# Performance work log

Hardware: AMD Instinct MI355X
Metric: run time of the kernel (lower is better)

The kernel has to match this reference:

```python
import jax, jax.numpy as jnp
import numpy as np

B, N, C, H, M, T, L = 2, 4096, 256, 8, 48, 10000, 256
CH = C // H
HID = 512  # mlp_ratio=2


def _ln(x, g, b, eps=1e-5):
    mu = x.mean(-1, keepdims=True)
    var = ((x - mu) ** 2).mean(-1, keepdims=True)
    return (x - mu) * jax.lax.rsqrt(var + eps) * g + b


def setup_inputs() -> dict:
    key = jax.random.key(0)
    ks = iter(jax.random.split(key, 40))
    nrm = lambda shape, s=0.02: jax.random.normal(next(ks), shape, jnp.float32) * s
    return dict(
        feat=jax.random.normal(next(ks), (B, N, C), jnp.float32),
        memory=jax.random.normal(next(ks), (B, L, C), jnp.float32),
        member_idx=jax.random.randint(next(ks), (B, N, M), 0, N),
        cluster_mask=jax.random.randint(next(ks), (B, N, M), 0, 2, jnp.int32),
        pe_idx=jax.random.randint(next(ks), (B, N, M), 0, T),
        global_attn=0,
        pre_table=jax.random.normal(next(ks), (T, 5), jnp.float32),
        Wq=nrm((C, C)), bq=jnp.zeros(C), Wkv=nrm((C, 2 * C)), bkv=jnp.zeros(2 * C),
        blank_k=nrm((C,), 1.0), blank_v=nrm((C,), 1.0),
        Wpe=nrm((5, H)), bpe=jnp.zeros(H),
        Wproj=nrm((C, C)), bproj=jnp.zeros(C),
        g1=jnp.ones(C), be1=jnp.zeros(C), g2=jnp.ones(C), be2=jnp.zeros(C),
        xWq=nrm((C, C)), xbq=jnp.zeros(C), xWk=nrm((C, C)), xbk=jnp.zeros(C),
        xWv=nrm((C, C)), xbv=jnp.zeros(C), xWo=nrm((C, C)), xbo=jnp.zeros(C),
        xg=jnp.ones(C), xbe=jnp.zeros(C),
        W1=nrm((C, HID)), bf1=jnp.zeros(HID), W2=nrm((HID, C)), bf2=jnp.zeros(C),
    )


def _cluster_attn(x, member_idx, cluster_mask, pe_idx, pre_table,
                  Wq, bq, Wkv, bkv, blank_k, blank_v, Wpe, bpe, Wproj, bproj):
    b, n, c = x.shape
    scale = CH ** -0.5
    q = ((x @ Wq + bq) * scale).reshape(b, n, H, CH).transpose(0, 2, 1, 3)  # bhnc
    kv = (x @ Wkv + bkv).reshape(b, n, H, 2, CH)
    k = kv[..., 0, :].transpose(0, 2, 1, 3)  # bhnc
    v = kv[..., 1, :].transpose(0, 2, 1, 3)  # bhnc
    # CLUSTENQK: gather per-token neighborhood keys, dot with q -> b h n m
    gather = jax.vmap(lambda t, idx: t[:, idx, :])  # (h,n,c),(n,m)->(h,n,m,c)
    k_g = gather(k, member_idx)
    attn = jnp.einsum('bhnc,bhnmc->bhnm', q, k_g)
    # positional embedding table lookup
    pe_table = pre_table @ Wpe + bpe                 # T x H
    pos = pe_table[pe_idx].transpose(0, 3, 1, 2)     # b h n m
    attn = attn + pos
    maskf = cluster_mask.astype(attn.dtype)[:, None]  # b 1 n m
    attn = attn + (1.0 - maskf) * -100.0
    blank_attn = jnp.einsum('bhnc,hc->bhn', q, blank_k.reshape(H, CH))[..., None]
    p = jax.nn.softmax(jnp.concatenate([attn, blank_attn], axis=-1), axis=-1)
    pa, pb = p[..., :-1], p[..., -1:]
    # CLUSTENAV: gather values, weighted sum
    v_g = gather(v, member_idx)
    out = jnp.einsum('bhnm,bhnmc->bhnc', pa, v_g)
    out = out + pb * blank_v.reshape(1, H, 1, CH)
    out = out.transpose(0, 2, 1, 3).reshape(b, n, c)
    return out @ Wproj + bproj


def _cross_attn(tgt, memory, xWq, xbq, xWk, xbk, xWv, xbv, xWo, xbo, xg, xbe):
    b, n, c = tgt.shape
    t2 = _ln(tgt, xg, xbe)  # normalize_before=True
    q = (t2 @ xWq + xbq).reshape(b, n, H, CH).transpose(0, 2, 1, 3) * (CH ** -0.5)
    k = (memory @ xWk + xbk).reshape(b, -1, H, CH).transpose(0, 2, 1, 3)
    v = (memory @ xWv + xbv).reshape(b, -1, H, CH).transpose(0, 2, 1, 3)
    p = jax.nn.softmax(jnp.einsum('bhnc,bhlc->bhnl', q, k), axis=-1)
    o = jnp.einsum('bhnl,bhlc->bhnc', p, v).transpose(0, 2, 1, 3).reshape(b, n, c)
    return tgt + (o @ xWo + xbo)


def reference(feat, memory, member_idx, cluster_mask, pe_idx, global_attn, pre_table,
              Wq, bq, Wkv, bkv, blank_k, blank_v, Wpe, bpe, Wproj, bproj,
              g1, be1, g2, be2,
              xWq, xbq, xWk, xbk, xWv, xbv, xWo, xbo, xg, xbe,
              W1, bf1, W2, bf2):
    # global_attn is a static flag; this reference covers the local-cluster path
    assert global_attn == 0
    # local cluster attention with pre-norm residual (drop_path/layer_scale disabled)
    feat = feat + _cluster_attn(_ln(feat, g1, be1), member_idx, cluster_mask, pe_idx,
                                pre_table, Wq, bq, Wkv, bkv, blank_k, blank_v,
                                Wpe, bpe, Wproj, bproj)
    # cross attention to memory (pre-norm, residual inside)
    feat = _cross_attn(feat, memory, xWq, xbq, xWk, xbk, xWv, xbv, xWo, xbo, xg, xbe)
    # MLP block
    h = jax.nn.gelu(_ln(feat, g2, be2) @ W1 + bf1, approximate=False)
    feat = feat + (h @ W2 + bf2)
    return feat
```

## Files before the change

kernel.cpp:

```cpp
#include <hip/hip_runtime.h>
#include <hip/hip_bf16.h>
#include <math.h>

#define BB 2
#define NN 4096
#define CC 256
#define HH 8
#define MM 48
#define TT 10000
#define LL 256
#define CHDIM 32
#define HIDD 512
#define ROWS (BB*NN)

typedef __attribute__((ext_vector_type(8))) short bf16x8;
typedef __attribute__((ext_vector_type(4))) float f32x4;

static __device__ __forceinline__ short f2bf(float x) {
    __hip_bfloat16 h = __float2bfloat16(x);
    return *reinterpret_cast<short*>(&h);
}
static __device__ __forceinline__ float bf2f(short s) {
    unsigned int u = ((unsigned int)(unsigned short)s) << 16;
    union { unsigned int u; float f; } c; c.u = u;
    return c.f;
}

__global__ void prep_misc_kernel(const float* __restrict__ pre, const float* __restrict__ Wpe,
                                 const float* __restrict__ bpe, float* __restrict__ pet,
                                 const float* __restrict__ bq, const float* __restrict__ bkv,
                                 const float* __restrict__ xbk, const float* __restrict__ xbv,
                                 const float* __restrict__ xbq, float scale,
                                 float* __restrict__ bqkv, float* __restrict__ xbkv,
                                 float* __restrict__ xbqS,
                                 const float* __restrict__ memory, __hip_bfloat16* __restrict__ memBf) {
    int bid = blockIdx.x, tid = threadIdx.x;
    if (bid < 313) {
        int i = bid * 256 + tid;
        if (i >= TT * HH) return;
        int t = i / HH, h = i % HH;
        float s = bpe[h];
        #pragma unroll
        for (int j = 0; j < 5; ++j) s += pre[t * 5 + j] * Wpe[j * HH + h];
        pet[i] = s;
    } else if (bid < 319) {
        int i = (bid - 313) * 256 + tid;
        if (i < 256) bqkv[i] = bq[i] * scale;
        else if (i < 768) bqkv[i] = bkv[i - 256];
        else if (i < 1024) xbkv[i - 768] = xbk[i - 768];
        else if (i < 1280) xbkv[256 + i - 1024] = xbv[i - 1024];
        else if (i < 1536) xbqS[i - 1280] = xbq[i - 1280] * scale;
    } else {
        int i = (bid - 319) * 256 + tid;
        if (i < 131072) memBf[i] = __float2bfloat16(memory[i]);
    }
}

struct WtDesc { const float* src; __hip_bfloat16* dst; int K; int N; int tile0; float scl; };
struct WtArgs { WtDesc d[9]; };
__global__ __launch_bounds__(256) void wtrans_kernel(WtArgs a) {
    __shared__ float tile[32][33];
    int bid = blockIdx.x;
    int mi = 0;
    #pragma unroll
    for (int i = 1; i < 9; ++i) if (bid >= a.d[i].tile0) mi = i;
    WtDesc dsc = a.d[mi];
    int t = bid - dsc.tile0;
    int tiles_n = dsc.N >> 5;
    int k0 = (t / tiles_n) * 32, n0 = (t % tiles_n) * 32;
    int tx = threadIdx.x & 31, ty = threadIdx.x >> 5;
    #pragma unroll
    for (int i = 0; i < 32; i += 8)
        tile[ty + i][tx] = dsc.src[(size_t)(k0 + ty + i) * dsc.N + n0 + tx];
    __syncthreads();
    #pragma unroll
    for (int i = 0; i < 32; i += 8)
        dsc.dst[(size_t)(n0 + ty + i) * dsc.K + k0 + tx] = __float2bfloat16(tile[tx][ty + i] * dsc.scl);
}

__global__ __launch_bounds__(256) void ln_kernel(const float* __restrict__ in,
                                                 const float* __restrict__ g,
                                                 const float* __restrict__ b,
                                                 __hip_bfloat16* __restrict__ out) {
    int row = blockIdx.x;
    int tid = threadIdx.x;
    float v = in[(size_t)row * CC + tid];
    __shared__ float r1[4], r2[4];
    float s = v;
    #pragma unroll
    for (int off = 32; off; off >>= 1) s += __shfl_xor(s, off, 64);
    if ((tid & 63) == 0) r1[tid >> 6] = s;
    __syncthreads();
    float mu = (r1[0] + r1[1] + r1[2] + r1[3]) * (1.0f / 256.0f);
    float d = v - mu;
    float s2 = d * d;
    #pragma unroll
    for (int off = 32; off; off >>= 1) s2 += __shfl_xor(s2, off, 64);
    if ((tid & 63) == 0) r2[tid >> 6] = s2;
    __syncthreads();
    float var = (r2[0] + r2[1] + r2[2] + r2[3]) * (1.0f / 256.0f);
    float rs = rsqrtf(var + 1e-5f);
    out[(size_t)row * CC + tid] = __float2bfloat16(d * rs * g[tid] + b[tid]);
}

#define GBM 128
#define GBN 64
#define GBK 64
#define LDA 72
template<int ACT, int OUTBF>
__global__ __launch_bounds__(256) void mfma_gemm_kernel(
    const __hip_bfloat16* __restrict__ A,
    const __hip_bfloat16* __restrict__ BT,
    const float* __restrict__ bias,
    void* __restrict__ outv,
    const float* __restrict__ residual,
    int M, int N, int K) {
    __shared__ short As[GBM * LDA];
    __shared__ short Bs[GBN * LDA];
    int tid = threadIdx.x;
    int lane = tid & 63, wid = tid >> 6;
    int wr = wid >> 1, wc = wid & 1;
    int row0 = blockIdx.y * GBM, col0 = blockIdx.x * GBN;
    int lr = lane & 15, lk = lane >> 4;
    f32x4 acc[4][2] = {};
    for (int kt = 0; kt < K; kt += GBK) {
        #pragma unroll
        for (int i = 0; i < 4; ++i) {
            int flat = tid + i * 256;
            int r = flat >> 3, kc = (flat & 7) * 8;
            *(bf16x8*)&As[r * LDA + kc] = *(const bf16x8*)(A + (size_t)(row0 + r) * K + kt + kc);
        }
        #pragma unroll
        for (int i = 0; i < 2; ++i) {
            int flat = tid + i * 256;
            int r = flat >> 3, kc = (flat & 7) * 8;
            *(bf16x8*)&Bs[r * LDA + kc] = *(const bf16x8*)(BT + (size_t)(col0 + r) * K + kt + kc);
        }
        __syncthreads();
        #pragma unroll
        for (int ks = 0; ks < 2; ++ks) {
            bf16x8 bfr[2];
            #pragma unroll
            for (int n = 0; n < 2; ++n)
                bfr[n] = *(const bf16x8*)&Bs[(wc * 32 + n * 16 + lr) * LDA + ks * 32 + lk * 8];
            #pragma unroll
            for (int m = 0; m < 4; ++m) {
                bf16x8 afr = *(const bf16x8*)&As[(wr * 64 + m * 16 + lr) * LDA + ks * 32 + lk * 8];
                #pragma unroll
                for (int n = 0; n < 2; ++n)
                    acc[m][n] = __builtin_amdgcn_mfma_f32_16x16x32_bf16(afr, bfr[n], acc[m][n], 0, 0, 0);
            }
        }
        __syncthreads();
    }
    float bv[2];
    #pragma unroll
    for (int n = 0; n < 2; ++n) bv[n] = bias[col0 + wc * 32 + n * 16 + lr];
    #pragma unroll
    for (int m = 0; m < 4; ++m) {
        #pragma unroll
        for (int n = 0; n < 2; ++n) {
            int col = col0 + wc * 32 + n * 16 + lr;
            #pragma unroll
            for (int r = 0; r < 4; ++r) {
                int row = row0 + wr * 64 + m * 16 + lk * 4 + r;
                float v = acc[m][n][r] + bv[n];
                if (ACT == 1) v = 0.5f * v * (1.0f + erff(v * 0.70710678118654752f));
                size_t oi = (size_t)row * N + col;
                if (residual) v += residual[oi];
                if (OUTBF) ((__hip_bfloat16*)outv)[oi] = __float2bfloat16(v);
                else ((float*)outv)[oi] = v;
            }
        }
    }
}

#define KVSTR 520
__global__ __launch_bounds__(512) void cluster_attn_kernel(
    const __hip_bfloat16* __restrict__ qkvh,
    const int* __restrict__ member_idx, const int* __restrict__ cluster_mask,
    const int* __restrict__ pe_idx, const float* __restrict__ pet,
    const float* __restrict__ blank_k, const float* __restrict__ blank_v,
    __hip_bfloat16* __restrict__ outp) {
    const short* qkv = (const short*)qkvh;
    __shared__ short s_kv[48 * KVSTR];
    __shared__ float s_q[256];
    __shared__ int   s_i[48];
    int tid = threadIdx.x;
    int row = blockIdx.x;
    int b = row >> 12;

    if (tid < MM) s_i[tid] = member_idx[(size_t)row * MM + tid];
    if (tid >= 256) s_q[tid - 256] = bf2f(qkv[(size_t)row * 768 + (tid - 256)]);
    __syncthreads();

    {
        int w = tid >> 6, l = tid & 63;
        #pragma unroll
        for (int r = 0; r < 6; ++r) {
            int m = w + r * 8;
            int im = s_i[m];
            bf16x8 v8 = *(const bf16x8*)(qkv + ((size_t)(b * NN + im)) * 768 + 256 + l * 8);
            *(bf16x8*)&s_kv[m * KVSTR + l * 8] = v8;
        }
    }
    __syncthreads();

    int h = tid >> 6, lane = tid & 63;
    const float* qf = s_q + h * CHDIM;
    float e = 0.0f;
    if (lane < MM) {
        const short* krow = s_kv + lane * KVSTR + h * 64;
        float d = pet[(size_t)pe_idx[(size_t)row * MM + lane] * HH + h];
        if (cluster_mask[(size_t)row * MM + lane] == 0) d -= 100.0f;
        #pragma unroll
        for (int c8 = 0; c8 < 4; ++c8) {
            bf16x8 kk = *(const bf16x8*)(krow + c8 * 8);
            d += qf[c8 * 8 + 0] * bf2f(kk[0]) + qf[c8 * 8 + 1] * bf2f(kk[1])
               + qf[c8 * 8 + 2] * bf2f(kk[2]) + qf[c8 * 8 + 3] * bf2f(kk[3])
               + qf[c8 * 8 + 4] * bf2f(kk[4]) + qf[c8 * 8 + 5] * bf2f(kk[5])
               + qf[c8 * 8 + 6] * bf2f(kk[6]) + qf[c8 * 8 + 7] * bf2f(kk[7]);
        }
        e = __expf(d);
    } else if (lane == MM) {
        const float* bk = blank_k + h * CHDIM;
        float d = 0.0f;
        #pragma unroll
        for (int c = 0; c < CHDIM; ++c) d += qf[c] * bk[c];
        e = __expf(d);
    }
    float ssum = e;
    #pragma unroll
    for (int off = 32; off; off >>= 1) ssum += __shfl_xor(ssum, off, 64);
    float p = e / ssum;
    float p48 = __shfl(p, MM, 64);

    int mg = lane >> 3, cq = lane & 7;
    float a0 = 0.f, a1 = 0.f, a2 = 0.f, a3 = 0.f;
    #pragma unroll
    for (int it = 0; it < 6; ++it) {
        int m = it * 8 + mg;
        float pm = __shfl(p, m, 64);
        const short* vp = s_kv + m * KVSTR + h * 64 + 32 + cq * 4;
        ushort4 vv = *(const ushort4*)vp;
        a0 += pm * bf2f(vv.x); a1 += pm * bf2f(vv.y);
        a2 += pm * bf2f(vv.z); a3 += pm * bf2f(vv.w);
    }
    #pragma unroll
    for (int off = 8; off < 64; off <<= 1) {
        a0 += __shfl_xor(a0, off, 64);
        a1 += __shfl_xor(a1, off, 64);
        a2 += __shfl_xor(a2, off, 64);
        a3 += __shfl_xor(a3, off, 64);
    }
    if (lane < 8) {
        const float* bvp = blank_v + h * CHDIM + cq * 4;
        a0 += p48 * bvp[0]; a1 += p48 * bvp[1]; a2 += p48 * bvp[2]; a3 += p48 * bvp[3];
        ushort4 o4;
        o4.x = (unsigned short)f2bf(a0); o4.y = (unsigned short)f2bf(a1);
        o4.z = (unsigned short)f2bf(a2); o4.w = (unsigned short)f2bf(a3);
        *(ushort4*)((unsigned short*)outp + (size_t)row * CC + h * CHDIM + cq * 4) = o4;
    }
}

#define KSLD 40
#define PVLD 264
__global__ __launch_bounds__(256) void cross_attn_kernel(
    const __hip_bfloat16* __restrict__ xq,
    const __hip_bfloat16* __restrict__ xkvh,
    __hip_bfloat16* __restrict__ o) {
    const short* xkv = (const short*)xkvh;
    extern __shared__ short lds[];
    short* Ks = lds;
    short* Vt = lds + 256 * KSLD;
    short* Ps = Vt + 32 * PVLD;
    int tid = threadIdx.x, lane = tid & 63, w = tid >> 6;
    int tile = blockIdx.x, h = blockIdx.y, b = blockIdx.z;
    int lr = lane & 15, g = lane >> 4;

    #pragma unroll
    for (int p = 0; p < 8; ++p) {
        int l = p * 32 + (tid >> 3);
        int c4 = (tid & 7) * 4;
        const short* kvrow = xkv + ((size_t)(b * LL + l)) * 512 + h * CHDIM;
        ushort4 kk = *(const ushort4*)(kvrow + c4);
        *(ushort4*)&Ks[l * KSLD + c4] = kk;
        ushort4 vv = *(const ushort4*)(kvrow + 256 + c4);
        Vt[(c4 + 0) * PVLD + l] = vv.x;
        Vt[(c4 + 1) * PVLD + l] = vv.y;
        Vt[(c4 + 2) * PVLD + l] = vv.z;
        Vt[(c4 + 3) * PVLD + l] = vv.w;
    }
    __syncthreads();

    int qrow = b * NN + tile * 64 + w * 16 + lr;
    bf16x8 afr = *(const bf16x8*)(xq + (size_t)qrow * CC + h * CHDIM + g * 8);
    f32x4 s[16];
    #pragma unroll
    for (int t = 0; t < 16; ++t) {
        bf16x8 kb = *(const bf16x8*)&Ks[(t * 16 + lr) * KSLD + g * 8];
        s[t] = __builtin_amdgcn_mfma_f32_16x16x32_bf16(afr, kb, (f32x4){0.f,0.f,0.f,0.f}, 0, 0, 0);
    }
    float rs[4] = {0.f, 0.f, 0.f, 0.f};
    #pragma unroll
    for (int t = 0; t < 16; ++t)
        #pragma unroll
        for (int r = 0; r < 4; ++r) { float e = __expf(s[t][r]); s[t][r] = e; rs[r] += e; }
    #pragma unroll
    for (int off = 1; off < 16; off <<= 1)
        #pragma unroll
        for (int r = 0; r < 4; ++r) rs[r] += __shfl_xor(rs[r], off, 64);
    short* Pw = Ps + w * 16 * PVLD;
    #pragma unroll
    for (int t = 0; t < 16; ++t)
        #pragma unroll
        for (int r = 0; r < 4; ++r)
            Pw[(g * 4 + r) * PVLD + t * 16 + lr] = f2bf(s[t][r]);
    f32x4 oacc[2] = {};
    #pragma unroll
    for (int kc = 0; kc < 8; ++kc) {
        bf16x8 pa = *(const bf16x8*)&Pw[lr * PVLD + kc * 32 + g * 8];
        #pragma unroll
        for (int n = 0; n < 2; ++n) {
            bf16x8 vb = *(const bf16x8*)&Vt[(n * 16 + lr) * PVLD + kc * 32 + g * 8];
            oacc[n] = __builtin_amdgcn_mfma_f32_16x16x32_bf16(pa, vb, oacc[n], 0, 0, 0);
        }
    }
    float inv[4];
    #pragma unroll
    for (int r = 0; r < 4; ++r) inv[r] = 1.0f / rs[r];
    #pragma unroll
    for (int n = 0; n < 2; ++n)
        #pragma unroll
        for (int r = 0; r < 4; ++r) {
            int orow = b * NN + tile * 64 + w * 16 + g * 4 + r;
            o[(size_t)orow * CC + h * CHDIM + n * 16 + lr] = __float2bfloat16(oacc[n][r] * inv[r]);
        }
}

extern "C" void kernel_launch(void* const* d_in, const int* in_sizes, int n_in,
                              void* d_out, int out_size, void* d_ws, size_t ws_size,
                              hipStream_t stream) {
    const float* feat        = (const float*)d_in[0];
    const float* memory      = (const float*)d_in[1];
    const int*   member_idx  = (const int*)d_in[2];
    const int*   cluster_mask= (const int*)d_in[3];
    const int*   pe_idx      = (const int*)d_in[4];
    const float* pre_table   = (const float*)d_in[6];
    const float* Wq    = (const float*)d_in[7];
    const float* bq    = (const float*)d_in[8];
    const float* Wkv   = (const float*)d_in[9];
    const float* bkv   = (const float*)d_in[10];
    const float* blank_k = (const float*)d_in[11];
    const float* blank_v = (const float*)d_in[12];
    const float* Wpe   = (const float*)d_in[13];
    const float* bpe   = (const float*)d_in[14];
    const float* Wproj = (const float*)d_in[15];
    const float* bproj = (const float*)d_in[16];
    const float* g1    = (const float*)d_in[17];
    const float* be1   = (const float*)d_in[18];
    const float* g2    = (const float*)d_in[19];
    const float* be2   = (const float*)d_in[20];
    const float* xWq   = (const float*)d_in[21];
    const float* xbq   = (const float*)d_in[22];
    const float* xWk   = (const float*)d_in[23];
    const float* xbk   = (const float*)d_in[24];
    const float* xWv   = (const float*)d_in[25];
    const float* xbv   = (const float*)d_in[26];
    const float* xWo   = (const float*)d_in[27];
    const float* xbo   = (const float*)d_in[28];
    const float* xg    = (const float*)d_in[29];
    const float* xbe   = (const float*)d_in[30];
    const float* W1    = (const float*)d_in[31];
    const float* bf1   = (const float*)d_in[32];
    const float* W2    = (const float*)d_in[33];
    const float* bf2   = (const float*)d_in[34];
    float* out = (float*)d_out;
    float* ws  = (float*)d_ws;

    __hip_bfloat16* qkvBf = (__hip_bfloat16*)ws;
    __hip_bfloat16* xqBf  = (__hip_bfloat16*)ws;
    __hip_bfloat16* xkvBf = (__hip_bfloat16*)(ws + 3145728);
    __hip_bfloat16* hBf   = (__hip_bfloat16*)(ws + 3276800);
    float* feat1F = ws + 5373952;
    __hip_bfloat16* aBf   = (__hip_bfloat16*)(ws + 7471104);
    __hip_bfloat16* oBf   = (__hip_bfloat16*)(ws + 8519680);
    __hip_bfloat16* WqkvT = (__hip_bfloat16*)(ws + 9568256);
    __hip_bfloat16* WprojT= (__hip_bfloat16*)(ws + 9666560);
    __hip_bfloat16* xWqT  = (__hip_bfloat16*)(ws + 9699328);
    __hip_bfloat16* xWoT  = (__hip_bfloat16*)(ws + 9732096);
    __hip_bfloat16* xWkvT = (__hip_bfloat16*)(ws + 9764864);
    __hip_bfloat16* W1T   = (__hip_bfloat16*)(ws + 9830400);
    __hip_bfloat16* W2T   = (__hip_bfloat16*)(ws + 9895936);
    __hip_bfloat16* memBf = (__hip_bfloat16*)(ws + 9961472);
    float* pet   = ws + 10027008;
    float* bqkv  = ws + 10107008;
    float* xbkv  = ws + 10107776;
    float* xbqS  = ws + 10108288;

    const float scale = 0.17677669529663689f;

    prep_misc_kernel<<<831, 256, 0, stream>>>(pre_table, Wpe, bpe, pet,
                                              bq, bkv, xbk, xbv, xbq, scale,
                                              bqkv, xbkv, xbqS, memory, memBf);
    WtArgs wa;
    wa.d[0] = { Wq,    WqkvT,          256, 256, 0,   scale };
    wa.d[1] = { Wkv,   WqkvT + 65536,  256, 512, 64,  1.0f };
    wa.d[2] = { Wproj, WprojT,         256, 256, 192, 1.0f };
    wa.d[3] = { xWq,   xWqT,           256, 256, 256, scale };
    wa.d[4] = { xWk,   xWkvT,          256, 256, 320, 1.0f };
    wa.d[5] = { xWv,   xWkvT + 65536,  256, 256, 384, 1.0f };
    wa.d[6] = { xWo,   xWoT,           256, 256, 448, 1.0f };
    wa.d[7] = { W1,    W1T,            256, 512, 512, 1.0f };
    wa.d[8] = { W2,    W2T,            512, 256, 640, 1.0f };
    wtrans_kernel<<<768, 256, 0, stream>>>(wa);

    ln_kernel<<<ROWS, 256, 0, stream>>>(feat, g1, be1, aBf);
    mfma_gemm_kernel<0,1><<<dim3(12, 64), 256, 0, stream>>>(aBf, WqkvT, bqkv, qkvBf, nullptr, ROWS, 768, 256);
    cluster_attn_kernel<<<ROWS, 512, 0, stream>>>(qkvBf, member_idx, cluster_mask, pe_idx, pet, blank_k, blank_v, oBf);
    mfma_gemm_kernel<0,0><<<dim3(4, 64), 256, 0, stream>>>(oBf, WprojT, bproj, feat1F, feat, ROWS, 256, 256);
    ln_kernel<<<ROWS, 256, 0, stream>>>(feat1F, xg, xbe, aBf);
    mfma_gemm_kernel<0,1><<<dim3(4, 64), 256, 0, stream>>>(aBf, xWqT, xbqS, xqBf, nullptr, ROWS, 256, 256);
    mfma_gemm_kernel<0,1><<<dim3(8, 4), 256, 0, stream>>>(memBf, xWkvT, xbkv, xkvBf, nullptr, 512, 512, 256);
    {
        size_t xlds = (256 * KSLD + 32 * PVLD + 4 * 16 * PVLD) * sizeof(short);
        cross_attn_kernel<<<dim3(NN / 64, HH, BB), 256, xlds, stream>>>(xqBf, xkvBf, oBf);
    }
    mfma_gemm_kernel<0,0><<<dim3(4, 64), 256, 0, stream>>>(oBf, xWoT, xbo, out, feat1F, ROWS, 256, 256);
    ln_kernel<<<ROWS, 256, 0, stream>>>(out, g2, be2, aBf);
    mfma_gemm_kernel<1,1><<<dim3(8, 64), 256, 0, stream>>>(aBf, W1T, bf1, hBf, nullptr, ROWS, HIDD, 256);
    mfma_gemm_kernel<0,0><<<dim3(4, 64), 256, 0, stream>>>(hBf, W2T, bf2, out, out, ROWS, 256, HIDD);
}
```

Before: 182.0 us.

## Merge prep launches, fuse cross-attn Q/KV GEMMs, vectorize layernorm, stage PE/mask

Folds the weight-transpose and misc-prep kernels into one launch, and runs the cross-attention Q and memory KV projections as a single dual-GEMM launch. It also rewrites layernorm to one wave per row using float4 loads with no LDS reductions. In cluster attention, the positional-bias and mask lookups move into shared memory once per token, so the 8 heads no longer issue redundant global gathers. Together these aim to cut launch count, barrier overhead and repeated global loads. The dual-GEMM grid adds idle early-exit blocks.

```diff
diff --git a/kernel.cpp b/kernel.cpp
--- a/kernel.cpp
+++ b/kernel.cpp
@@ -26,15 +26,38 @@
     return c.f;
 }
 
-__global__ void prep_misc_kernel(const float* __restrict__ pre, const float* __restrict__ Wpe,
-                                 const float* __restrict__ bpe, float* __restrict__ pet,
-                                 const float* __restrict__ bq, const float* __restrict__ bkv,
-                                 const float* __restrict__ xbk, const float* __restrict__ xbv,
-                                 const float* __restrict__ xbq, float scale,
-                                 float* __restrict__ bqkv, float* __restrict__ xbkv,
-                                 float* __restrict__ xbqS,
-                                 const float* __restrict__ memory, __hip_bfloat16* __restrict__ memBf) {
+struct WtDesc { const float* src; __hip_bfloat16* dst; int K; int N; int tile0; float scl; };
+struct WtArgs { WtDesc d[9]; };
+
+__global__ __launch_bounds__(256) void prep_all_kernel(WtArgs a,
+    const float* __restrict__ pre, const float* __restrict__ Wpe,
+    const float* __restrict__ bpe, float* __restrict__ pet,
+    const float* __restrict__ bq, const float* __restrict__ bkv,
+    const float* __restrict__ xbk, const float* __restrict__ xbv,
+    const float* __restrict__ xbq, float scale,
+    float* __restrict__ bqkv, float* __restrict__ xbkv, float* __restrict__ xbqS,
+    const float* __restrict__ memory, __hip_bfloat16* __restrict__ memBf) {
+    __shared__ float tile[32][33];
     int bid = blockIdx.x, tid = threadIdx.x;
+    if (bid < 768) {
+        int mi = 0;
+        #pragma unroll
+        for (int i = 1; i < 9; ++i) if (bid >= a.d[i].tile0) mi = i;
+        WtDesc dsc = a.d[mi];
+        int t = bid - dsc.tile0;
+        int tiles_n = dsc.N >> 5;
+        int k0 = (t / tiles_n) * 32, n0 = (t % tiles_n) * 32;
+        int tx = tid & 31, ty = tid >> 5;
+        #pragma unroll
+        for (int i = 0; i < 32; i += 8)
+            tile[ty + i][tx] = dsc.src[(size_t)(k0 + ty + i) * dsc.N + n0 + tx];
+        __syncthreads();
+        #pragma unroll
+        for (int i = 0; i < 32; i += 8)
+            dsc.dst[(size_t)(n0 + ty + i) * dsc.K + k0 + tx] = __float2bfloat16(tile[tx][ty + i] * dsc.scl);
+        return;
+    }
+    bid -= 768;
     if (bid < 313) {
         int i = bid * 256 + tid;
         if (i >= TT * HH) return;
@@ -56,51 +79,30 @@
     }
 }
 
-struct WtDesc { const float* src; __hip_bfloat16* dst; int K; int N; int tile0; float scl; };
-struct WtArgs { WtDesc d[9]; };
-__global__ __launch_bounds__(256) void wtrans_kernel(WtArgs a) {
-    __shared__ float tile[32][33];
-    int bid = blockIdx.x;
-    int mi = 0;
-    #pragma unroll
-    for (int i = 1; i < 9; ++i) if (bid >= a.d[i].tile0) mi = i;
-    WtDesc dsc = a.d[mi];
-    int t = bid - dsc.tile0;
-    int tiles_n = dsc.N >> 5;
-    int k0 = (t / tiles_n) * 32, n0 = (t % tiles_n) * 32;
-    int tx = threadIdx.x & 31, ty = threadIdx.x >> 5;
-    #pragma unroll
-    for (int i = 0; i < 32; i += 8)
-        tile[ty + i][tx] = dsc.src[(size_t)(k0 + ty + i) * dsc.N + n0 + tx];
-    __syncthreads();
-    #pragma unroll
-    for (int i = 0; i < 32; i += 8)
-        dsc.dst[(size_t)(n0 + ty + i) * dsc.K + k0 + tx] = __float2bfloat16(tile[tx][ty + i] * dsc.scl);
-}
-
 __global__ __launch_bounds__(256) void ln_kernel(const float* __restrict__ in,
                                                  const float* __restrict__ g,
                                                  const float* __restrict__ b,
                                                  __hip_bfloat16* __restrict__ out) {
-    int row = blockIdx.x;
-    int tid = threadIdx.x;
-    float v = in[(size_t)row * CC + tid];
-    __shared__ float r1[4], r2[4];
-    float s = v;
+    int wave = threadIdx.x >> 6, lane = threadIdx.x & 63;
+    int row = blockIdx.x * 4 + wave;
+    float4 v = ((const float4*)(in + (size_t)row * CC))[lane];
+    float s = (v.x + v.y) + (v.z + v.w);
     #pragma unroll
     for (int off = 32; off; off >>= 1) s += __shfl_xor(s, off, 64);
-    if ((tid & 63) == 0) r1[tid >> 6] = s;
-    __syncthreads();
-    float mu = (r1[0] + r1[1] + r1[2] + r1[3]) * (1.0f / 256.0f);
-    float d = v - mu;
-    float s2 = d * d;
+    float mu = s * (1.0f / 256.0f);
+    float dx = v.x - mu, dy = v.y - mu, dz = v.z - mu, dw = v.w - mu;
+    float s2 = (dx * dx + dy * dy) + (dz * dz + dw * dw);
     #pragma unroll
     for (int off = 32; off; off >>= 1) s2 += __shfl_xor(s2, off, 64);
-    if ((tid & 63) == 0) r2[tid >> 6] = s2;
-    __syncthreads();
-    float var = (r2[0] + r2[1] + r2[2] + r2[3]) * (1.0f / 256.0f);
-    float rs = rsqrtf(var + 1e-5f);
-    out[(size_t)row * CC + tid] = __float2bfloat16(d * rs * g[tid] + b[tid]);
+    float rs = rsqrtf(s2 * (1.0f / 256.0f) + 1e-5f);
+    float4 g4 = ((const float4*)g)[lane];
+    float4 b4 = ((const float4*)b)[lane];
+    ushort4 o4;
+    o4.x = (unsigned short)f2bf(dx * rs * g4.x + b4.x);
+    o4.y = (unsigned short)f2bf(dy * rs * g4.y + b4.y);
+    o4.z = (unsigned short)f2bf(dz * rs * g4.z + b4.z);
+    o4.w = (unsigned short)f2bf(dw * rs * g4.w + b4.w);
+    *(ushort4*)((unsigned short*)out + (size_t)row * CC + lane * 4) = o4;
 }
 
 #define GBM 128
@@ -108,19 +110,13 @@
 #define GBK 64
 #define LDA 72
 template<int ACT, int OUTBF>
-__global__ __launch_bounds__(256) void mfma_gemm_kernel(
-    const __hip_bfloat16* __restrict__ A,
-    const __hip_bfloat16* __restrict__ BT,
-    const float* __restrict__ bias,
-    void* __restrict__ outv,
-    const float* __restrict__ residual,
-    int M, int N, int K) {
-    __shared__ short As[GBM * LDA];
-    __shared__ short Bs[GBN * LDA];
+__device__ __forceinline__ void gemm_body(short* As, short* Bs,
+    const __hip_bfloat16* __restrict__ A, const __hip_bfloat16* __restrict__ BT,
+    const float* __restrict__ bias, void* __restrict__ outv,
+    const float* __restrict__ residual, int N, int K, int row0, int col0) {
     int tid = threadIdx.x;
     int lane = tid & 63, wid = tid >> 6;
     int wr = wid >> 1, wc = wid & 1;
-    int row0 = blockIdx.y * GBM, col0 = blockIdx.x * GBN;
     int lr = lane & 15, lk = lane >> 4;
     f32x4 acc[4][2] = {};
     for (int kt = 0; kt < K; kt += GBK) {
@@ -175,6 +171,35 @@
     }
 }
 
+template<int ACT, int OUTBF>
+__global__ __launch_bounds__(256) void mfma_gemm_kernel(
+    const __hip_bfloat16* __restrict__ A, const __hip_bfloat16* __restrict__ BT,
+    const float* __restrict__ bias, void* __restrict__ outv,
+    const float* __restrict__ residual, int M, int N, int K) {
+    __shared__ short As[GBM * LDA];
+    __shared__ short Bs[GBN * LDA];
+    gemm_body<ACT, OUTBF>(As, Bs, A, BT, bias, outv, residual, N, K,
+                          blockIdx.y * GBM, blockIdx.x * GBN);
+}
+
+struct GemmPair {
+    const __hip_bfloat16 *A1, *B1; const float* bias1; void* out1;
+    const __hip_bfloat16 *A2, *B2; const float* bias2; void* out2;
+};
+__global__ __launch_bounds__(256) void dual_gemm_kernel(GemmPair p) {
+    __shared__ short As[GBM * LDA];
+    __shared__ short Bs[GBN * LDA];
+    if (blockIdx.x < 4) {
+        gemm_body<0, 1>(As, Bs, p.A1, p.B1, p.bias1, p.out1, nullptr, 256, 256,
+                        blockIdx.y * GBM, blockIdx.x * GBN);
+    } else {
+        int row0 = blockIdx.y * GBM;
+        if (row0 >= 512) return;
+        gemm_body<0, 1>(As, Bs, p.A2, p.B2, p.bias2, p.out2, nullptr, 512, 256,
+                        row0, (blockIdx.x - 4) * GBN);
+    }
+}
+
 #define KVSTR 520
 __global__ __launch_bounds__(512) void cluster_attn_kernel(
     const __hip_bfloat16* __restrict__ qkvh,
@@ -184,25 +209,32 @@
     __hip_bfloat16* __restrict__ outp) {
     const short* qkv = (const short*)qkvh;
     __shared__ short s_kv[48 * KVSTR];
+    __shared__ float s_pm[48 * 9];
     __shared__ float s_q[256];
-    __shared__ int   s_i[48];
     int tid = threadIdx.x;
     int row = blockIdx.x;
     int b = row >> 12;
 
-    if (tid < MM) s_i[tid] = member_idx[(size_t)row * MM + tid];
-    if (tid >= 256) s_q[tid - 256] = bf2f(qkv[(size_t)row * 768 + (tid - 256)]);
-    __syncthreads();
-
     {
         int w = tid >> 6, l = tid & 63;
         #pragma unroll
         for (int r = 0; r < 6; ++r) {
             int m = w + r * 8;
-            int im = s_i[m];
+            int im = member_idx[(size_t)row * MM + m];
             bf16x8 v8 = *(const bf16x8*)(qkv + ((size_t)(b * NN + im)) * 768 + 256 + l * 8);
             *(bf16x8*)&s_kv[m * KVSTR + l * 8] = v8;
         }
+    }
+    if (tid < MM) {
+        float mb = cluster_mask[(size_t)row * MM + tid] ? 0.0f : -100.0f;
+        int pidx = pe_idx[(size_t)row * MM + tid];
+        const float4* pr = (const float4*)(pet + (size_t)pidx * 8);
+        float4 p0 = pr[0], p1 = pr[1];
+        float* dst = &s_pm[tid * 9];
+        dst[0] = p0.x + mb; dst[1] = p0.y + mb; dst[2] = p0.z + mb; dst[3] = p0.w + mb;
+        dst[4] = p1.x + mb; dst[5] = p1.y + mb; dst[6] = p1.z + mb; dst[7] = p1.w + mb;
+    } else if (tid >= 256) {
+        s_q[tid - 256] = bf2f(qkv[(size_t)row * 768 + (tid - 256)]);
     }
     __syncthreads();
 
@@ -211,8 +243,7 @@
     float e = 0.0f;
     if (lane < MM) {
         const short* krow = s_kv + lane * KVSTR + h * 64;
-        float d = pet[(size_t)pe_idx[(size_t)row * MM + lane] * HH + h];
-        if (cluster_mask[(size_t)row * MM + lane] == 0) d -= 100.0f;
+        float d = s_pm[lane * 9 + h];
         #pragma unroll
         for (int c8 = 0; c8 < 4; ++c8) {
             bf16x8 kk = *(const bf16x8*)(krow + c8 * 8);
@@ -400,9 +431,6 @@
 
     const float scale = 0.17677669529663689f;
 
-    prep_misc_kernel<<<831, 256, 0, stream>>>(pre_table, Wpe, bpe, pet,
-                                              bq, bkv, xbk, xbv, xbq, scale,
-                                              bqkv, xbkv, xbqS, memory, memBf);
     WtArgs wa;
     wa.d[0] = { Wq,    WqkvT,          256, 256, 0,   scale };
     wa.d[1] = { Wkv,   WqkvT + 65536,  256, 512, 64,  1.0f };
@@ -413,21 +441,27 @@
     wa.d[6] = { xWo,   xWoT,           256, 256, 448, 1.0f };
     wa.d[7] = { W1,    W1T,            256, 512, 512, 1.0f };
     wa.d[8] = { W2,    W2T,            512, 256, 640, 1.0f };
-    wtrans_kernel<<<768, 256, 0, stream>>>(wa);
-
-    ln_kernel<<<ROWS, 256, 0, stream>>>(feat, g1, be1, aBf);
+    prep_all_kernel<<<768 + 831, 256, 0, stream>>>(wa, pre_table, Wpe, bpe, pet,
+                                                   bq, bkv, xbk, xbv, xbq, scale,
+                                                   bqkv, xbkv, xbqS, memory, memBf);
+
+    ln_kernel<<<ROWS / 4, 256, 0, stream>>>(feat, g1, be1, aBf);
     mfma_gemm_kernel<0,1><<<dim3(12, 64), 256, 0, stream>>>(aBf, WqkvT, bqkv, qkvBf, nullptr, ROWS, 768, 256);
     cluster_attn_kernel<<<ROWS, 512, 0, stream>>>(qkvBf, member_idx, cluster_mask, pe_idx, pet, blank_k, blank_v, oBf);
     mfma_gemm_kernel<0,0><<<dim3(4, 64), 256, 0, stream>>>(oBf, WprojT, bproj, feat1F, feat, ROWS, 256, 256);
-    ln_kernel<<<ROWS, 256, 0, stream>>>(feat1F, xg, xbe, aBf);
-    mfma_gemm_kernel<0,1><<<dim3(4, 64), 256, 0, stream>>>(aBf, xWqT, xbqS, xqBf, nullptr, ROWS, 256, 256);
-    mfma_gemm_kernel<0,1><<<dim3(8, 4), 256, 0, stream>>>(memBf, xWkvT, xbkv, xkvBf, nullptr, 512, 512, 256);
+    ln_kernel<<<ROWS / 4, 256, 0, stream>>>(feat1F, xg, xbe, aBf);
+    {
+        GemmPair gp;
+        gp.A1 = aBf;   gp.B1 = xWqT;  gp.bias1 = xbqS; gp.out1 = xqBf;
+        gp.A2 = memBf; gp.B2 = xWkvT; gp.bias2 = xbkv; gp.out2 = xkvBf;
+        dual_gemm_kernel<<<dim3(12, 64), 256, 0, stream>>>(gp);
+    }
     {
         size_t xlds = (256 * KSLD + 32 * PVLD + 4 * 16 * PVLD) * sizeof(short);
         cross_attn_kernel<<<dim3(NN / 64, HH, BB), 256, xlds, stream>>>(xqBf, xkvBf, oBf);
     }
     mfma_gemm_kernel<0,0><<<dim3(4, 64), 256, 0, stream>>>(oBf, xWoT, xbo, out, feat1F, ROWS, 256, 256);
-    ln_kernel<<<ROWS, 256, 0, stream>>>(out, g2, be2, aBf);
+    ln_kernel<<<ROWS / 4, 256, 0, stream>>>(out, g2, be2, aBf);
     mfma_gemm_kernel<1,1><<<dim3(8, 64), 256, 0, stream>>>(aBf, W1T, bf1, hBf, nullptr, ROWS, HIDD, 256);
     mfma_gemm_kernel<0,0><<<dim3(4, 64), 256, 0, stream>>>(hBf, W2T, bf2, out, out, ROWS, 256, HIDD);
 }
```

Measured after the change: 162.2 us. 10.9% less time.
